# Performance work log

Hardware: AMD Instinct MI355X
Metric: run time of the kernel (lower is better)

## Reference

```python
import jax, jax.numpy as jnp
import numpy as np

NUM_EXPERTS = 8
TOP_K = 2

def setup_inputs() -> dict:
    key = jax.random.key(0)
    ks = jax.random.split(key, 7)
    T, D, H, E = 4096, 1024, 4096, NUM_EXPERTS
    s_in = (2.0 / (D + H)) ** 0.5   # xavier-ish scale for W1
    s_out = (2.0 / (H + D)) ** 0.5
    return {
        "x": jax.random.normal(ks[0], (T, D), jnp.float32),
        "Wg": jax.random.normal(ks[1], (D, E), jnp.float32) * 0.02,
        "bg": jnp.zeros((E,), jnp.float32),
        "W1": jax.random.normal(ks[2], (E, D, H), jnp.float32) * s_in,
        "b1": jnp.zeros((E, H), jnp.float32),
        "W2": jax.random.normal(ks[3], (E, H, D), jnp.float32) * s_out,
        "b2": jnp.zeros((E, D), jnp.float32),
    }

def reference(x, Wg, bg, W1, b1, W2, b2):
    # x: [T, D]; gate over E experts
    gate = jax.nn.softmax(x @ Wg + bg, axis=-1)            # [T, E]
    _, top_idx = jax.lax.top_k(gate, TOP_K)                # [T, K]
    # mask[t, e] = True iff expert e is among top-k for token t
    mask = jnp.any(top_idx[:, :, None] == jnp.arange(NUM_EXPERTS)[None, None, :], axis=1)
    combine_w = jnp.where(mask, gate, 0.0)                 # [T, E]
    # out = sum_e combine_w[:, e] * MLP_e(x); non-selected tokens get weight 0
    out = jnp.zeros_like(x)
    for e in range(NUM_EXPERTS):  # small fixed expert loop
        h = jax.nn.relu(x @ W1[e] + b1[e])                 # [T, H]
        y = h @ W2[e] + b2[e]                              # [T, D]
        out = out + combine_w[:, e:e + 1] * y
    return out
```

## Files before the change

kernel.cpp:

```cpp
#include <hip/hip_runtime.h>
#include <stdint.h>

#define T_TOK 4096
#define DDIM  1024
#define HDIM  4096
#define NEXP  8
#define MAXTILES 72

typedef short s16x8  __attribute__((ext_vector_type(8)));
typedef short s16x4  __attribute__((ext_vector_type(4)));
typedef float f32x4t __attribute__((ext_vector_type(4)));

#define GLOAD16(gp, lp) __builtin_amdgcn_global_load_lds( \
    (const __attribute__((address_space(1))) unsigned int*)(gp), \
    (__attribute__((address_space(3))) unsigned int*)(lp), 16, 0, 0)
#define SB0 __builtin_amdgcn_sched_barrier(0)

__device__ __forceinline__ unsigned short f2b(float f){
  unsigned int u = __float_as_uint(f);
  u += 0x7fffu + ((u >> 16) & 1u);
  return (unsigned short)(u >> 16);
}

__device__ __forceinline__ s16x8 lds_frag(const unsigned short* base, int row, int colElem){
  int byte = row*64 + ((colElem*2) ^ (((row >> 1) & 3) << 4));
  return *(const s16x8*)((const char*)base + byte);
}

__global__ void gate_kernel(const float* __restrict__ x, const float* __restrict__ Wg,
                            const float* __restrict__ bg,
                            int* __restrict__ topk_e, float* __restrict__ topk_w){
  const int t = blockIdx.x;
  const int lane = threadIdx.x;
  const float* xr = x + (size_t)t * DDIM;
  float acc[NEXP];
  #pragma unroll
  for (int e = 0; e < NEXP; ++e) acc[e] = 0.f;
  #pragma unroll 4
  for (int it = 0; it < DDIM/64; ++it){
    int i = it*64 + lane;
    float xi = xr[i];
    const float4* wr = (const float4*)(Wg + (size_t)i * NEXP);
    float4 w0 = wr[0], w1 = wr[1];
    acc[0] += xi*w0.x; acc[1] += xi*w0.y; acc[2] += xi*w0.z; acc[3] += xi*w0.w;
    acc[4] += xi*w1.x; acc[5] += xi*w1.y; acc[6] += xi*w1.z; acc[7] += xi*w1.w;
  }
  #pragma unroll
  for (int e = 0; e < NEXP; ++e){
    float v = acc[e];
    #pragma unroll
    for (int off = 32; off > 0; off >>= 1) v += __shfl_xor(v, off, 64);
    acc[e] = v;
  }
  if (lane == 0){
    float l[NEXP], m = -1e30f;
    #pragma unroll
    for (int e = 0; e < NEXP; ++e){ l[e] = acc[e] + bg[e]; m = fmaxf(m, l[e]); }
    float p[NEXP], s = 0.f;
    #pragma unroll
    for (int e = 0; e < NEXP; ++e){ p[e] = expf(l[e] - m); s += p[e]; }
    float inv = 1.f / s;
    int a1 = 0; float v1 = -1.f;
    #pragma unroll
    for (int e = 0; e < NEXP; ++e){ p[e] *= inv; if (p[e] > v1){ v1 = p[e]; a1 = e; } }
    int a2 = -1; float v2 = -1.f;
    #pragma unroll
    for (int e = 0; e < NEXP; ++e){ if (e == a1) continue; if (p[e] > v2){ v2 = p[e]; a2 = e; } }
    topk_e[2*t]   = a1; topk_w[2*t]   = v1;
    topk_e[2*t+1] = a2; topk_w[2*t+1] = v2;
  }
}

__global__ void route_count(const int* __restrict__ topk_e, const float* __restrict__ topk_w,
                            int* __restrict__ expertList, float* __restrict__ pairW,
                            int* __restrict__ counts){
  const int e = blockIdx.x;
  const int tid = threadIdx.x;
  __shared__ int pfx[256];
  __shared__ int base_s;
  if (tid == 0) base_s = 0;
  __syncthreads();
  for (int c = 0; c < T_TOK/256; ++c){
    int t = c*256 + tid;
    int e0 = topk_e[2*t], e1 = topk_e[2*t+1];
    int sel = 0; float w = 0.f;
    if (e0 == e){ sel = 1; w = topk_w[2*t]; }
    else if (e1 == e){ sel = 1; w = topk_w[2*t+1]; }
    pfx[tid] = sel;
    __syncthreads();
    for (int off = 1; off < 256; off <<= 1){
      int v = (tid >= off) ? pfx[tid - off] : 0;
      __syncthreads();
      pfx[tid] += v;
      __syncthreads();
    }
    if (sel){
      int pos = base_s + pfx[tid] - 1;
      expertList[e*T_TOK + pos] = t;
      pairW[e*T_TOK + pos] = w;
    }
    __syncthreads();
    if (tid == 0) base_s += pfx[255];
    __syncthreads();
  }
  if (tid == 0) counts[e] = base_s;
}

__global__ void plan_kernel(const int* __restrict__ counts, int* __restrict__ nTiles,
                            int* __restrict__ tileExpert, int* __restrict__ tileStart){
  if (blockIdx.x != 0 || threadIdx.x != 0) return;
  int nt = 0;
  for (int e = 0; e < NEXP; ++e){
    int c = counts[e];
    int tcount = (c + 127) >> 7;
    for (int i = 0; i < tcount; ++i){ tileExpert[nt] = e; tileStart[nt] = i*128; ++nt; }
  }
  *nTiles = nt;
}

__global__ void conv_x(const float* __restrict__ x, unsigned short* __restrict__ xb){
  int i = (blockIdx.x*256 + threadIdx.x)*4;
  float4 v = *(const float4*)(x + i);
  s16x4 o;
  o[0] = (short)f2b(v.x); o[1] = (short)f2b(v.y);
  o[2] = (short)f2b(v.z); o[3] = (short)f2b(v.w);
  *(s16x4*)(xb + i) = o;
}

__global__ __launch_bounds__(256)
void transpose_w(const float* __restrict__ W, unsigned short* __restrict__ Wt,
                 int K, int N){
  const int e = blockIdx.z;
  const float* Wb = W + (size_t)e*K*N;
  unsigned short* Wtb = Wt + (size_t)e*K*N;
  const int n0 = blockIdx.x*64, k0 = blockIdx.y*64;
  __shared__ unsigned short t[64][72];
  const int r  = threadIdx.x >> 4;
  const int c4 = (threadIdx.x & 15) * 4;
  #pragma unroll
  for (int i = 0; i < 4; ++i){
    int k = r + i*16;
    float4 v = *(const float4*)(Wb + (size_t)(k0+k)*N + n0 + c4);
    t[c4+0][k] = f2b(v.x); t[c4+1][k] = f2b(v.y);
    t[c4+2][k] = f2b(v.z); t[c4+3][k] = f2b(v.w);
  }
  __syncthreads();
  const int kk = (threadIdx.x & 7) * 8;
  #pragma unroll
  for (int i = 0; i < 2; ++i){
    int n = (threadIdx.x >> 3) + i*32;
    s16x8 v;
    #pragma unroll
    for (int j = 0; j < 8; ++j) v[j] = (short)t[n][kk+j];
    *(s16x8*)(Wtb + (size_t)(n0+n)*K + k0 + kk) = v;
  }
}

template<int LAYER, int KS>
__global__ __launch_bounds__(256, 4)
void moe_gemm(const unsigned short* __restrict__ Abf,
              const unsigned short* __restrict__ Wt,
              const float* __restrict__ bias,
              const int* __restrict__ nTilesPtr,
              const int* __restrict__ tileExpert,
              const int* __restrict__ tileStart,
              const int* __restrict__ counts,
              const int* __restrict__ expertList,
              const float* __restrict__ pairW,
              unsigned short* __restrict__ Hout,
              float* __restrict__ out)
{
  constexpr int KD = (LAYER == 1) ? DDIM : HDIM;
  constexpr int ND = (LAYER == 1) ? HDIM : DDIM;
  constexpr int NB = ND / 128;
  constexpr int NTfull = KD / 32;

  const int nwg = gridDim.x;
  const int b   = blockIdx.x;
  const int q8 = nwg >> 3, r8 = nwg & 7;
  const int xcd = b & 7, ii = b >> 3;
  const int lin = (xcd < r8 ? xcd*(q8+1) : r8*(q8+1) + (xcd-r8)*q8) + ii;
  const int tile = lin / NB;
  const int n0   = (lin % NB) * 128;
  const int kz   = blockIdx.y;

  if (tile >= *nTilesPtr) return;
  const int e   = tileExpert[tile];
  const int ts  = tileStart[tile];
  const int cnt = counts[e];
  const int tid  = threadIdx.x;
  const int lane = tid & 63;
  const int wave = tid >> 6;
  const int wm = (wave >> 1) * 64;
  const int wn = (wave & 1) * 64;

  __shared__ __align__(16) unsigned short As[2][128][32];
  __shared__ __align__(16) unsigned short Bs[2][128][32];
  __shared__ int   tokenBuf[128];
  __shared__ float wBuf[128];

  if (tid < 128){
    int pos = ts + tid;
    int tok = 0; float w = 0.f;
    if (pos < cnt){ tok = expertList[e*T_TOK + pos]; w = pairW[e*T_TOK + pos]; }
    tokenBuf[tid] = tok; wBuf[tid] = w;
  }
  __syncthreads();

  const int srow = tid >> 2;
  const int slot = (tid & 3) ^ ((tid >> 3) & 3);
  const int koff = slot * 8;
  const unsigned short* gA[2];
  const unsigned short* gB[2];
  #pragma unroll
  for (int g = 0; g < 2; ++g){
    const int row = g*64 + srow;
    if (LAYER == 1) gA[g] = Abf + (size_t)tokenBuf[row]*DDIM + koff;
    else            gA[g] = Abf + (size_t)(tile*128 + row)*HDIM + koff;
    gB[g] = Wt + ((size_t)e*ND + n0 + row)*KD + koff;
  }

  auto STAGE = [&](int buf, int ko){
    unsigned short* la = &As[buf][wave*16][0];
    unsigned short* lb = &Bs[buf][wave*16][0];
    #pragma unroll
    for (int g = 0; g < 2; ++g){
      GLOAD16(gA[g] + ko, la + g*2048);
      GLOAD16(gB[g] + ko, lb + g*2048);
    }
  };

  f32x4t acc[4][4] = {};
  const int fr = lane & 15;
  const int fq = lane >> 4;

  const int kt0 = (kz * NTfull) / KS;
  const int kt1 = ((kz + 1) * NTfull) / KS;
  const int NTl = kt1 - kt0;

  STAGE(0, kt0*32);

  int cur = 0;
  for (int t = 0; t < NTl; ++t){
    if (t + 1 < NTl){
      STAGE(cur ^ 1, (kt0 + t + 1)*32);
      SB0; asm volatile("s_waitcnt vmcnt(4)" ::: "memory");
    } else {
      SB0; asm volatile("s_waitcnt vmcnt(0)" ::: "memory");
    }
    __builtin_amdgcn_s_barrier();
    SB0;

    const unsigned short* Ab = &As[cur][0][0];
    const unsigned short* Bb = &Bs[cur][0][0];
    s16x8 bfr[4], afr[4];
    #pragma unroll
    for (int nf = 0; nf < 4; ++nf) bfr[nf] = lds_frag(Bb, wn + nf*16 + fr, fq*8);
    #pragma unroll
    for (int mf = 0; mf < 4; ++mf) afr[mf] = lds_frag(Ab, wm + mf*16 + fr, fq*8);
    #pragma unroll
    for (int mf = 0; mf < 4; ++mf)
      #pragma unroll
      for (int nf = 0; nf < 4; ++nf)
        acc[mf][nf] = __builtin_amdgcn_mfma_f32_16x16x32_bf16(afr[mf], bfr[nf], acc[mf][nf], 0, 0, 0);

    SB0;
    __builtin_amdgcn_s_barrier();
    SB0;
    cur ^= 1;
  }

  const int rbase = wm + fq*4;
  const int cbase = wn + fr;
  if (LAYER == 1){
    #pragma unroll
    for (int mf = 0; mf < 4; ++mf){
      #pragma unroll
      for (int nf = 0; nf < 4; ++nf){
        int c = cbase + nf*16;
        float bsv = bias[e*HDIM + n0 + c];
        #pragma unroll
        for (int j = 0; j < 4; ++j){
          int rr = rbase + mf*16 + j;
          float v = fmaxf(acc[mf][nf][j] + bsv, 0.f);
          __builtin_nontemporal_store((unsigned short)f2b(v),
              &Hout[(size_t)(tile*128 + rr)*HDIM + n0 + c]);
        }
      }
    }
  } else {
    #pragma unroll
    for (int mf = 0; mf < 4; ++mf){
      #pragma unroll
      for (int j = 0; j < 4; ++j){
        int rr = rbase + mf*16 + j;
        if (ts + rr < cnt){
          int tok = tokenBuf[rr];
          float w = wBuf[rr];
          #pragma unroll
          for (int nf = 0; nf < 4; ++nf){
            int c = cbase + nf*16;
            float v = acc[mf][nf][j];
            if (kz == 0) v += bias[e*DDIM + n0 + c];
            atomicAdd(out + (size_t)tok*DDIM + n0 + c, w * v);
          }
        }
      }
    }
  }
}

extern "C" void kernel_launch(void* const* d_in, const int* in_sizes, int n_in,
                              void* d_out, int out_size, void* d_ws, size_t ws_size,
                              hipStream_t stream){
  const float* x  = (const float*)d_in[0];
  const float* Wg = (const float*)d_in[1];
  const float* bg = (const float*)d_in[2];
  const float* W1 = (const float*)d_in[3];
  const float* b1 = (const float*)d_in[4];
  const float* W2 = (const float*)d_in[5];
  const float* b2 = (const float*)d_in[6];
  float* out = (float*)d_out;

  char* p = (char*)d_ws;
  int*   topk_e     = (int*)p;   p += (size_t)T_TOK*2*sizeof(int);
  float* topk_w     = (float*)p; p += (size_t)T_TOK*2*sizeof(float);
  int*   counts     = (int*)p;   p += 8*sizeof(int);
  int*   nTiles     = (int*)p;   p += 8*sizeof(int);
  int*   tileExpert = (int*)p;   p += 128*sizeof(int);
  int*   tileStart  = (int*)p;   p += 128*sizeof(int);
  int*   expertList = (int*)p;   p += (size_t)NEXP*T_TOK*sizeof(int);
  float* pairW      = (float*)p; p += (size_t)NEXP*T_TOK*sizeof(float);
  p = (char*)(((uintptr_t)p + 255) & ~(uintptr_t)255);
  unsigned short* xb = (unsigned short*)p;
  p += (size_t)T_TOK*DDIM*sizeof(unsigned short);
  p = (char*)(((uintptr_t)p + 255) & ~(uintptr_t)255);
  unsigned short* Wtbuf = (unsigned short*)p;
  p += (size_t)NEXP*DDIM*HDIM*sizeof(unsigned short);
  p = (char*)(((uintptr_t)p + 255) & ~(uintptr_t)255);
  unsigned short* Hact = (unsigned short*)p;

  hipMemsetAsync(d_out, 0, (size_t)T_TOK*DDIM*sizeof(float), stream);
  gate_kernel<<<T_TOK, 64, 0, stream>>>(x, Wg, bg, topk_e, topk_w);
  route_count<<<NEXP, 256, 0, stream>>>(topk_e, topk_w, expertList, pairW, counts);
  plan_kernel<<<1, 1, 0, stream>>>(counts, nTiles, tileExpert, tileStart);
  conv_x<<<T_TOK*DDIM/1024, 256, 0, stream>>>(x, xb);

  transpose_w<<<dim3(HDIM/64, DDIM/64, NEXP), 256, 0, stream>>>(W1, Wtbuf, DDIM, HDIM);
  moe_gemm<1,1><<<dim3(MAXTILES*(HDIM/128), 1), 256, 0, stream>>>(
      xb, Wtbuf, b1, nTiles, tileExpert, tileStart, counts, expertList, pairW, Hact, nullptr);

  transpose_w<<<dim3(DDIM/64, HDIM/64, NEXP), 256, 0, stream>>>(W2, Wtbuf, HDIM, DDIM);
  moe_gemm<2,2><<<dim3(MAXTILES*(DDIM/128), 2), 256, 0, stream>>>(
      Hact, Wtbuf, b2, nTiles, tileExpert, tileStart, counts, expertList, pairW, nullptr, out);
}
```

Baseline: 387.1 us.

## Widen MoE GEMM tiles to 128x256 with 8 waves and fuse x conversion into gate

The grouped expert GEMM now uses 512-thread blocks with 8 waves covering a 128x256 output tile, so each staged A tile is reused across twice as many output columns. Split-K for the second layer goes from 2 to 4 to keep enough blocks. The separate fp32-to-bf16 conversion kernel for x is folded into the gate kernel, which already reads x. The costs are more LDS per block, fewer resident blocks, and more atomic or partial accumulation traffic from the wider split-K. The gate kernel's bf16 stores are narrow, uncoalesced-width writes.

Result: slower. 406.5 us (+5.0%).

```diff
diff --git a/kernel.cpp b/kernel.cpp
--- a/kernel.cpp
+++ b/kernel.cpp
@@ -29,10 +29,12 @@
 
 __global__ void gate_kernel(const float* __restrict__ x, const float* __restrict__ Wg,
                             const float* __restrict__ bg,
-                            int* __restrict__ topk_e, float* __restrict__ topk_w){
+                            int* __restrict__ topk_e, float* __restrict__ topk_w,
+                            unsigned short* __restrict__ xb){
   const int t = blockIdx.x;
   const int lane = threadIdx.x;
   const float* xr = x + (size_t)t * DDIM;
+  unsigned short* xbr = xb + (size_t)t * DDIM;
   float acc[NEXP];
   #pragma unroll
   for (int e = 0; e < NEXP; ++e) acc[e] = 0.f;
@@ -40,6 +42,7 @@
   for (int it = 0; it < DDIM/64; ++it){
     int i = it*64 + lane;
     float xi = xr[i];
+    xbr[i] = f2b(xi);
     const float4* wr = (const float4*)(Wg + (size_t)i * NEXP);
     float4 w0 = wr[0], w1 = wr[1];
     acc[0] += xi*w0.x; acc[1] += xi*w0.y; acc[2] += xi*w0.z; acc[3] += xi*w0.w;
@@ -118,15 +121,6 @@
   *nTiles = nt;
 }
 
-__global__ void conv_x(const float* __restrict__ x, unsigned short* __restrict__ xb){
-  int i = (blockIdx.x*256 + threadIdx.x)*4;
-  float4 v = *(const float4*)(x + i);
-  s16x4 o;
-  o[0] = (short)f2b(v.x); o[1] = (short)f2b(v.y);
-  o[2] = (short)f2b(v.z); o[3] = (short)f2b(v.w);
-  *(s16x4*)(xb + i) = o;
-}
-
 __global__ __launch_bounds__(256)
 void transpose_w(const float* __restrict__ W, unsigned short* __restrict__ Wt,
                  int K, int N){
@@ -157,7 +151,7 @@
 }
 
 template<int LAYER, int KS>
-__global__ __launch_bounds__(256, 4)
+__global__ __launch_bounds__(512, 3)
 void moe_gemm(const unsigned short* __restrict__ Abf,
               const unsigned short* __restrict__ Wt,
               const float* __restrict__ bias,
@@ -172,7 +166,7 @@
 {
   constexpr int KD = (LAYER == 1) ? DDIM : HDIM;
   constexpr int ND = (LAYER == 1) ? HDIM : DDIM;
-  constexpr int NB = ND / 128;
+  constexpr int NB = ND / 256;
   constexpr int NTfull = KD / 32;
 
   const int nwg = gridDim.x;
@@ -181,7 +175,7 @@
   const int xcd = b & 7, ii = b >> 3;
   const int lin = (xcd < r8 ? xcd*(q8+1) : r8*(q8+1) + (xcd-r8)*q8) + ii;
   const int tile = lin / NB;
-  const int n0   = (lin % NB) * 128;
+  const int n0   = (lin % NB) * 256;
   const int kz   = blockIdx.y;
 
   if (tile >= *nTilesPtr) return;
@@ -191,11 +185,11 @@
   const int tid  = threadIdx.x;
   const int lane = tid & 63;
   const int wave = tid >> 6;
-  const int wm = (wave >> 1) * 64;
-  const int wn = (wave & 1) * 64;
+  const int wm = (wave >> 2) * 64;
+  const int wn = (wave & 3) * 64;
 
   __shared__ __align__(16) unsigned short As[2][128][32];
-  __shared__ __align__(16) unsigned short Bs[2][128][32];
+  __shared__ __align__(16) unsigned short Bs[2][256][32];
   __shared__ int   tokenBuf[128];
   __shared__ float wBuf[128];
 
@@ -210,24 +204,22 @@
   const int srow = tid >> 2;
   const int slot = (tid & 3) ^ ((tid >> 3) & 3);
   const int koff = slot * 8;
-  const unsigned short* gA[2];
+  const unsigned short* gA;
   const unsigned short* gB[2];
-  #pragma unroll
-  for (int g = 0; g < 2; ++g){
-    const int row = g*64 + srow;
-    if (LAYER == 1) gA[g] = Abf + (size_t)tokenBuf[row]*DDIM + koff;
-    else            gA[g] = Abf + (size_t)(tile*128 + row)*HDIM + koff;
-    gB[g] = Wt + ((size_t)e*ND + n0 + row)*KD + koff;
+  {
+    if (LAYER == 1) gA = Abf + (size_t)tokenBuf[srow]*DDIM + koff;
+    else            gA = Abf + (size_t)(tile*128 + srow)*HDIM + koff;
+    #pragma unroll
+    for (int g = 0; g < 2; ++g)
+      gB[g] = Wt + ((size_t)e*ND + n0 + g*128 + srow)*KD + koff;
   }
 
   auto STAGE = [&](int buf, int ko){
-    unsigned short* la = &As[buf][wave*16][0];
-    unsigned short* lb = &Bs[buf][wave*16][0];
-    #pragma unroll
-    for (int g = 0; g < 2; ++g){
-      GLOAD16(gA[g] + ko, la + g*2048);
-      GLOAD16(gB[g] + ko, lb + g*2048);
-    }
+    unsigned short* la = &As[buf][0][0] + wave*512;
+    unsigned short* lb = &Bs[buf][0][0] + wave*512;
+    GLOAD16(gA + ko, la);
+    GLOAD16(gB[0] + ko, lb);
+    GLOAD16(gB[1] + ko, lb + 4096);
   };
 
   f32x4t acc[4][4] = {};
@@ -244,7 +236,7 @@
   for (int t = 0; t < NTl; ++t){
     if (t + 1 < NTl){
       STAGE(cur ^ 1, (kt0 + t + 1)*32);
-      SB0; asm volatile("s_waitcnt vmcnt(4)" ::: "memory");
+      SB0; asm volatile("s_waitcnt vmcnt(3)" ::: "memory");
     } else {
       SB0; asm volatile("s_waitcnt vmcnt(0)" ::: "memory");
     }
@@ -341,16 +333,15 @@
   unsigned short* Hact = (unsigned short*)p;
 
   hipMemsetAsync(d_out, 0, (size_t)T_TOK*DDIM*sizeof(float), stream);
-  gate_kernel<<<T_TOK, 64, 0, stream>>>(x, Wg, bg, topk_e, topk_w);
+  gate_kernel<<<T_TOK, 64, 0, stream>>>(x, Wg, bg, topk_e, topk_w, xb);
   route_count<<<NEXP, 256, 0, stream>>>(topk_e, topk_w, expertList, pairW, counts);
   plan_kernel<<<1, 1, 0, stream>>>(counts, nTiles, tileExpert, tileStart);
-  conv_x<<<T_TOK*DDIM/1024, 256, 0, stream>>>(x, xb);
 
   transpose_w<<<dim3(HDIM/64, DDIM/64, NEXP), 256, 0, stream>>>(W1, Wtbuf, DDIM, HDIM);
-  moe_gemm<1,1><<<dim3(MAXTILES*(HDIM/128), 1), 256, 0, stream>>>(
+  moe_gemm<1,1><<<dim3(MAXTILES*(HDIM/256), 1), 512, 0, stream>>>(
       xb, Wtbuf, b1, nTiles, tileExpert, tileStart, counts, expertList, pairW, Hact, nullptr);
 
   transpose_w<<<dim3(DDIM/64, HDIM/64, NEXP), 256, 0, stream>>>(W2, Wtbuf, HDIM, DDIM);
-  moe_gemm<2,2><<<dim3(MAXTILES*(DDIM/128), 2), 256, 0, stream>>>(
+  moe_gemm<2,4><<<dim3(MAXTILES*(DDIM/256), 4), 512, 0, stream>>>(
       Hact, Wtbuf, b2, nTiles, tileExpert, tileStart, counts, expertList, pairW, nullptr, out);
 }
```

## Use 256x256 8-wave tiles for first expert GEMM and fuse x conversion into gate

Applied to the files above, without the earlier changes.

The first-layer expert GEMM moves from 128x128 tiles with BK=32 to a 512-thread 256x256 tile with BK=64. Its loads are staged in quarters interleaved with MFMA sub-blocks and raised wave priority, aiming at more data reuse and better load/compute overlap. Routing tiles become 256 tokens, and the second GEMM splits each 256-tile into two 128-row halves. The bf16 conversion of x is folded into the gate kernel, removing one launch and one read of x. The risks are more padding waste per expert with 256-row tiles, one workgroup per CU from LDS and register pressure, and uncoalesced 2-byte stores in the gate kernel.

Measured after the change: 406.5 us. 1.05x slower.

```diff
diff --git a/kernel.cpp b/kernel.cpp
--- a/kernel.cpp
+++ b/kernel.cpp
@@ -5,7 +5,8 @@
 #define DDIM  1024
 #define HDIM  4096
 #define NEXP  8
-#define MAXTILES 72
+#define MAXT256 40
+#define MAXT128 80
 
 typedef short s16x8  __attribute__((ext_vector_type(8)));
 typedef short s16x4  __attribute__((ext_vector_type(4)));
@@ -22,17 +23,23 @@
   return (unsigned short)(u >> 16);
 }
 
-__device__ __forceinline__ s16x8 lds_frag(const unsigned short* base, int row, int colElem){
+__device__ __forceinline__ s16x8 lds_frag32(const unsigned short* base, int row, int colElem){
   int byte = row*64 + ((colElem*2) ^ (((row >> 1) & 3) << 4));
   return *(const s16x8*)((const char*)base + byte);
 }
+__device__ __forceinline__ s16x8 lds_frag64(const unsigned short* base, int row, int colElem){
+  int byte = row*128 + ((colElem*2) ^ ((row & 7) << 4));
+  return *(const s16x8*)((const char*)base + byte);
+}
 
 __global__ void gate_kernel(const float* __restrict__ x, const float* __restrict__ Wg,
                             const float* __restrict__ bg,
-                            int* __restrict__ topk_e, float* __restrict__ topk_w){
+                            int* __restrict__ topk_e, float* __restrict__ topk_w,
+                            unsigned short* __restrict__ xb){
   const int t = blockIdx.x;
   const int lane = threadIdx.x;
   const float* xr = x + (size_t)t * DDIM;
+  unsigned short* xbr = xb + (size_t)t * DDIM;
   float acc[NEXP];
   #pragma unroll
   for (int e = 0; e < NEXP; ++e) acc[e] = 0.f;
@@ -40,6 +47,7 @@
   for (int it = 0; it < DDIM/64; ++it){
     int i = it*64 + lane;
     float xi = xr[i];
+    xbr[i] = f2b(xi);
     const float4* wr = (const float4*)(Wg + (size_t)i * NEXP);
     float4 w0 = wr[0], w1 = wr[1];
     acc[0] += xi*w0.x; acc[1] += xi*w0.y; acc[2] += xi*w0.z; acc[3] += xi*w0.w;
@@ -112,19 +120,10 @@
   int nt = 0;
   for (int e = 0; e < NEXP; ++e){
     int c = counts[e];
-    int tcount = (c + 127) >> 7;
-    for (int i = 0; i < tcount; ++i){ tileExpert[nt] = e; tileStart[nt] = i*128; ++nt; }
+    int tcount = (c + 255) >> 8;
+    for (int i = 0; i < tcount; ++i){ tileExpert[nt] = e; tileStart[nt] = i*256; ++nt; }
   }
   *nTiles = nt;
-}
-
-__global__ void conv_x(const float* __restrict__ x, unsigned short* __restrict__ xb){
-  int i = (blockIdx.x*256 + threadIdx.x)*4;
-  float4 v = *(const float4*)(x + i);
-  s16x4 o;
-  o[0] = (short)f2b(v.x); o[1] = (short)f2b(v.y);
-  o[2] = (short)f2b(v.z); o[3] = (short)f2b(v.w);
-  *(s16x4*)(xb + i) = o;
 }
 
 __global__ __launch_bounds__(256)
@@ -156,24 +155,20 @@
   }
 }
 
-template<int LAYER, int KS>
-__global__ __launch_bounds__(256, 4)
-void moe_gemm(const unsigned short* __restrict__ Abf,
-              const unsigned short* __restrict__ Wt,
-              const float* __restrict__ bias,
-              const int* __restrict__ nTilesPtr,
-              const int* __restrict__ tileExpert,
-              const int* __restrict__ tileStart,
-              const int* __restrict__ counts,
-              const int* __restrict__ expertList,
-              const float* __restrict__ pairW,
-              unsigned short* __restrict__ Hout,
-              float* __restrict__ out)
+__global__ __launch_bounds__(512, 1)
+void moe_gemm8(const unsigned short* __restrict__ Abf,
+               const unsigned short* __restrict__ Wt,
+               const float* __restrict__ bias,
+               const int* __restrict__ nTilesPtr,
+               const int* __restrict__ tileExpert,
+               const int* __restrict__ tileStart,
+               const int* __restrict__ counts,
+               const int* __restrict__ expertList,
+               unsigned short* __restrict__ Hout)
 {
-  constexpr int KD = (LAYER == 1) ? DDIM : HDIM;
-  constexpr int ND = (LAYER == 1) ? HDIM : DDIM;
-  constexpr int NB = ND / 128;
-  constexpr int NTfull = KD / 32;
+  constexpr int ND = HDIM;
+  constexpr int NB = ND / 256;
+  constexpr int NT = DDIM / 64;
 
   const int nwg = gridDim.x;
   const int b   = blockIdx.x;
@@ -181,8 +176,7 @@
   const int xcd = b & 7, ii = b >> 3;
   const int lin = (xcd < r8 ? xcd*(q8+1) : r8*(q8+1) + (xcd-r8)*q8) + ii;
   const int tile = lin / NB;
-  const int n0   = (lin % NB) * 128;
-  const int kz   = blockIdx.y;
+  const int n0   = (lin % NB) * 256;
 
   if (tile >= *nTilesPtr) return;
   const int e   = tileExpert[tile];
@@ -191,6 +185,177 @@
   const int tid  = threadIdx.x;
   const int lane = tid & 63;
   const int wave = tid >> 6;
+  const int wr = wave >> 2;
+  const int wc = wave & 3;
+
+  __shared__ __align__(16) unsigned short As[2][256][64];
+  __shared__ __align__(16) unsigned short Bs[2][256][64];
+  __shared__ int tokenBuf[256];
+
+  if (tid < 256){
+    int pos = ts + tid;
+    int tok = 0;
+    if (pos < cnt) tok = expertList[e*T_TOK + pos];
+    tokenBuf[tid] = tok;
+  }
+  __syncthreads();
+
+  const int srow = tid >> 3;
+  const int slot = (tid & 7) ^ (srow & 7);
+  const int koff = slot * 8;
+  const unsigned short* gA[4];
+  const unsigned short* gB[4];
+  #pragma unroll
+  for (int h = 0; h < 2; ++h)
+    #pragma unroll
+    for (int g = 0; g < 2; ++g){
+      const int row = h*128 + g*64 + srow;
+      gA[h*2+g] = Abf + (size_t)tokenBuf[row]*DDIM + koff;
+      gB[h*2+g] = Wt + ((size_t)e*ND + n0 + row)*DDIM + koff;
+    }
+
+  auto STAGE_HALF = [&](int buf, int which, int ko){
+    if (which < 2){
+      #pragma unroll
+      for (int g = 0; g < 2; ++g)
+        GLOAD16(gA[which*2+g] + ko, &As[buf][which*128 + g*64 + wave*8][0]);
+    } else {
+      const int h = which - 2;
+      #pragma unroll
+      for (int g = 0; g < 2; ++g)
+        GLOAD16(gB[h*2+g] + ko, &Bs[buf][h*128 + g*64 + wave*8][0]);
+    }
+  };
+
+  f32x4t acc[8][4] = {};
+  const int fr = lane & 15;
+  const int fq = lane >> 4;
+
+  #pragma unroll
+  for (int w = 0; w < 4; ++w) STAGE_HALF(0, w, 0);
+
+  int cur = 0;
+  for (int t = 0; t < NT; ++t){
+    const bool has_next = (t + 1 < NT);
+    const int ko_next = (t + 1) * 64;
+    const unsigned short* Ab = &As[cur][0][0];
+    const unsigned short* Bb = &Bs[cur][0][0];
+    s16x8 bfr[4][2];
+
+    if (has_next){
+      STAGE_HALF(cur^1, 0, ko_next);
+      SB0; asm volatile("s_waitcnt vmcnt(2)" ::: "memory");
+    } else {
+      SB0; asm volatile("s_waitcnt vmcnt(0)" ::: "memory");
+    }
+    __builtin_amdgcn_s_barrier();
+    SB0;
+    #pragma unroll
+    for (int nf = 0; nf < 4; ++nf)
+      #pragma unroll
+      for (int ks = 0; ks < 2; ++ks)
+        bfr[nf][ks] = lds_frag64(Bb, wc*64 + nf*16 + fr, ks*32 + fq*8);
+    {
+      s16x8 afr[2][2];
+      #pragma unroll
+      for (int i = 0; i < 2; ++i)
+        #pragma unroll
+        for (int ks = 0; ks < 2; ++ks)
+          afr[i][ks] = lds_frag64(Ab, wr*128 + i*16 + fr, ks*32 + fq*8);
+      __builtin_amdgcn_s_setprio(1);
+      #pragma unroll
+      for (int ks = 0; ks < 2; ++ks)
+        #pragma unroll
+        for (int i = 0; i < 2; ++i)
+          #pragma unroll
+          for (int nf = 0; nf < 4; ++nf)
+            acc[i][nf] = __builtin_amdgcn_mfma_f32_16x16x32_bf16(
+                afr[i][ks], bfr[nf][ks], acc[i][nf], 0, 0, 0);
+      __builtin_amdgcn_s_setprio(0);
+    }
+    SB0;
+    __builtin_amdgcn_s_barrier();
+    SB0;
+
+    #pragma unroll
+    for (int q = 1; q < 4; ++q){
+      if (has_next) STAGE_HALF(cur^1, q, ko_next);
+      s16x8 afr[2][2];
+      #pragma unroll
+      for (int i = 0; i < 2; ++i)
+        #pragma unroll
+        for (int ks = 0; ks < 2; ++ks)
+          afr[i][ks] = lds_frag64(Ab, wr*128 + q*32 + i*16 + fr, ks*32 + fq*8);
+      __builtin_amdgcn_s_setprio(1);
+      #pragma unroll
+      for (int ks = 0; ks < 2; ++ks)
+        #pragma unroll
+        for (int i = 0; i < 2; ++i)
+          #pragma unroll
+          for (int nf = 0; nf < 4; ++nf)
+            acc[q*2+i][nf] = __builtin_amdgcn_mfma_f32_16x16x32_bf16(
+                afr[i][ks], bfr[nf][ks], acc[q*2+i][nf], 0, 0, 0);
+      __builtin_amdgcn_s_setprio(0);
+      SB0;
+      __builtin_amdgcn_s_barrier();
+      SB0;
+    }
+    cur ^= 1;
+  }
+
+  const int rbase = wr*128 + fq*4;
+  const int cbase = wc*64 + fr;
+  #pragma unroll
+  for (int mf = 0; mf < 8; ++mf){
+    #pragma unroll
+    for (int nf = 0; nf < 4; ++nf){
+      int c = cbase + nf*16;
+      float bsv = bias[e*HDIM + n0 + c];
+      #pragma unroll
+      for (int j = 0; j < 4; ++j){
+        int rr = rbase + mf*16 + j;
+        float v = fmaxf(acc[mf][nf][j] + bsv, 0.f);
+        __builtin_nontemporal_store((unsigned short)f2b(v),
+            &Hout[(size_t)(tile*256 + rr)*HDIM + n0 + c]);
+      }
+    }
+  }
+}
+
+template<int KS>
+__global__ __launch_bounds__(256, 4)
+void moe_gemm2(const unsigned short* __restrict__ Abf,
+               const unsigned short* __restrict__ Wt,
+               const float* __restrict__ bias,
+               const int* __restrict__ nTilesPtr,
+               const int* __restrict__ tileExpert,
+               const int* __restrict__ tileStart,
+               const int* __restrict__ counts,
+               const int* __restrict__ expertList,
+               const float* __restrict__ pairW,
+               float* __restrict__ out)
+{
+  constexpr int KD = HDIM;
+  constexpr int ND = DDIM;
+  constexpr int NB = ND / 128;
+  constexpr int NTfull = KD / 32;
+
+  const int nwg = gridDim.x;
+  const int b   = blockIdx.x;
+  const int q8 = nwg >> 3, r8 = nwg & 7;
+  const int xcd = b & 7, ii = b >> 3;
+  const int lin = (xcd < r8 ? xcd*(q8+1) : r8*(q8+1) + (xcd-r8)*q8) + ii;
+  const int t128 = lin / NB;
+  const int n0   = (lin % NB) * 128;
+  const int kz   = blockIdx.y;
+
+  if ((t128 >> 1) >= *nTilesPtr) return;
+  const int e   = tileExpert[t128 >> 1];
+  const int ts  = tileStart[t128 >> 1] + (t128 & 1) * 128;
+  const int cnt = counts[e];
+  const int tid  = threadIdx.x;
+  const int lane = tid & 63;
+  const int wave = tid >> 6;
   const int wm = (wave >> 1) * 64;
   const int wn = (wave & 1) * 64;
 
@@ -215,8 +380,7 @@
   #pragma unroll
   for (int g = 0; g < 2; ++g){
     const int row = g*64 + srow;
-    if (LAYER == 1) gA[g] = Abf + (size_t)tokenBuf[row]*DDIM + koff;
-    else            gA[g] = Abf + (size_t)(tile*128 + row)*HDIM + koff;
+    gA[g] = Abf + (size_t)(t128*128 + row)*HDIM + koff;
     gB[g] = Wt + ((size_t)e*ND + n0 + row)*KD + koff;
   }
 
@@ -255,9 +419,9 @@
     const unsigned short* Bb = &Bs[cur][0][0];
     s16x8 bfr[4], afr[4];
     #pragma unroll
-    for (int nf = 0; nf < 4; ++nf) bfr[nf] = lds_frag(Bb, wn + nf*16 + fr, fq*8);
-    #pragma unroll
-    for (int mf = 0; mf < 4; ++mf) afr[mf] = lds_frag(Ab, wm + mf*16 + fr, fq*8);
+    for (int nf = 0; nf < 4; ++nf) bfr[nf] = lds_frag32(Bb, wn + nf*16 + fr, fq*8);
+    #pragma unroll
+    for (int mf = 0; mf < 4; ++mf) afr[mf] = lds_frag32(Ab, wm + mf*16 + fr, fq*8);
     #pragma unroll
     for (int mf = 0; mf < 4; ++mf)
       #pragma unroll
@@ -272,38 +436,20 @@
 
   const int rbase = wm + fq*4;
   const int cbase = wn + fr;
-  if (LAYER == 1){
-    #pragma unroll
-    for (int mf = 0; mf < 4; ++mf){
-      #pragma unroll
-      for (int nf = 0; nf < 4; ++nf){
-        int c = cbase + nf*16;
-        float bsv = bias[e*HDIM + n0 + c];
+  #pragma unroll
+  for (int mf = 0; mf < 4; ++mf){
+    #pragma unroll
+    for (int j = 0; j < 4; ++j){
+      int rr = rbase + mf*16 + j;
+      if (ts + rr < cnt){
+        int tok = tokenBuf[rr];
+        float w = wBuf[rr];
         #pragma unroll
-        for (int j = 0; j < 4; ++j){
-          int rr = rbase + mf*16 + j;
-          float v = fmaxf(acc[mf][nf][j] + bsv, 0.f);
-          __builtin_nontemporal_store((unsigned short)f2b(v),
-              &Hout[(size_t)(tile*128 + rr)*HDIM + n0 + c]);
-        }
-      }
-    }
-  } else {
-    #pragma unroll
-    for (int mf = 0; mf < 4; ++mf){
-      #pragma unroll
-      for (int j = 0; j < 4; ++j){
-        int rr = rbase + mf*16 + j;
-        if (ts + rr < cnt){
-          int tok = tokenBuf[rr];
-          float w = wBuf[rr];
-          #pragma unroll
-          for (int nf = 0; nf < 4; ++nf){
-            int c = cbase + nf*16;
-            float v = acc[mf][nf][j];
-            if (kz == 0) v += bias[e*DDIM + n0 + c];
-            atomicAdd(out + (size_t)tok*DDIM + n0 + c, w * v);
-          }
+        for (int nf = 0; nf < 4; ++nf){
+          int c = cbase + nf*16;
+          float v = acc[mf][nf][j];
+          if (kz == 0) v += bias[e*DDIM + n0 + c];
+          atomicAdd(out + (size_t)tok*DDIM + n0 + c, w * v);
         }
       }
     }
@@ -341,16 +487,15 @@
   unsigned short* Hact = (unsigned short*)p;
 
   hipMemsetAsync(d_out, 0, (size_t)T_TOK*DDIM*sizeof(float), stream);
-  gate_kernel<<<T_TOK, 64, 0, stream>>>(x, Wg, bg, topk_e, topk_w);
+  gate_kernel<<<T_TOK, 64, 0, stream>>>(x, Wg, bg, topk_e, topk_w, xb);
   route_count<<<NEXP, 256, 0, stream>>>(topk_e, topk_w, expertList, pairW, counts);
   plan_kernel<<<1, 1, 0, stream>>>(counts, nTiles, tileExpert, tileStart);
-  conv_x<<<T_TOK*DDIM/1024, 256, 0, stream>>>(x, xb);
 
   transpose_w<<<dim3(HDIM/64, DDIM/64, NEXP), 256, 0, stream>>>(W1, Wtbuf, DDIM, HDIM);
-  moe_gemm<1,1><<<dim3(MAXTILES*(HDIM/128), 1), 256, 0, stream>>>(
-      xb, Wtbuf, b1, nTiles, tileExpert, tileStart, counts, expertList, pairW, Hact, nullptr);
+  moe_gemm8<<<MAXT256*(HDIM/256), 512, 0, stream>>>(
+      xb, Wtbuf, b1, nTiles, tileExpert, tileStart, counts, expertList, Hact);
 
   transpose_w<<<dim3(DDIM/64, HDIM/64, NEXP), 256, 0, stream>>>(W2, Wtbuf, HDIM, DDIM);
-  moe_gemm<2,2><<<dim3(MAXTILES*(DDIM/128), 2), 256, 0, stream>>>(
-      Hact, Wtbuf, b2, nTiles, tileExpert, tileStart, counts, expertList, pairW, nullptr, out);
-}
+  moe_gemm2<2><<<dim3(MAXT128*(DDIM/128), 2), 256, 0, stream>>>(
+      Hact, Wtbuf, b2, nTiles, tileExpert, tileStart, counts, expertList, pairW, out);
+}
```
